# Optimization experiments

Measured on AMD Instinct MI355X. Metric: run time of the kernel, lower is better.

## Reference

```python
import jax, jax.numpy as jnp
from jax import lax
import numpy as np

IMG_CH = 3
C = 48            # total channels
HIDDEN = 256
FIRE_RATE = 0.5
DX_NOISE = 0.0
NEG_SLOPE = 0.01  # torch LeakyReLU default


def _dwconv(x_nchw, w):
    # depthwise 3x3 conv with reflect padding, w: [C,1,3,3]
    xp = jnp.pad(x_nchw, ((0, 0), (0, 0), (1, 1), (1, 1)), mode='reflect')
    return lax.conv_general_dilated(
        xp, w, window_strides=(1, 1), padding='VALID',
        feature_group_count=C,
        dimension_numbers=('NCHW', 'OIHW', 'NCHW'))


def setup_inputs() -> dict:
    key = jax.random.key(0)
    ks = jax.random.split(key, 6)
    x = jax.random.normal(ks[0], (8, 256, 256, C), dtype=jnp.float32)
    filt0 = jax.random.normal(ks[1], (C, 1, 3, 3), dtype=jnp.float32) * 0.1
    filt1 = jax.random.normal(ks[2], (C, 1, 3, 3), dtype=jnp.float32) * 0.1
    fan_in = 3 * C
    w1 = jax.random.normal(ks[3], (HIDDEN, 3 * C), dtype=jnp.float32) / np.sqrt(fan_in).astype(np.float32)
    b1 = jax.random.normal(ks[4], (HIDDEN,), dtype=jnp.float32) * 0.01
    # original zero-inits w2; randomized small so outputs/grads are nontrivial
    w2 = jax.random.normal(ks[5], (C, HIDDEN), dtype=jnp.float32) * 0.02
    return {"x": x, "filt0": filt0, "filt1": filt1, "w1": w1, "b1": b1, "w2": w2, "steps": 4}


def reference(x, filt0, filt1, w1, b1, w2, steps):
    ch_mask = (jnp.arange(C) >= IMG_CH).astype(x.dtype)  # immutable image channels
    rng = jax.random.key(42)
    for i in range(steps):
        xc = jnp.transpose(x, (0, 3, 1, 2))                       # [B,C,H,W]
        p = jnp.concatenate([xc, _dwconv(xc, filt0), _dwconv(xc, filt1)], axis=1)
        p = jnp.transpose(p, (0, 2, 3, 1))                        # [B,H,W,3C]
        h = jax.nn.leaky_relu(jnp.einsum('bhwf,of->bhwo', p, w1) + b1, NEG_SLOPE)
        d = jnp.einsum('bhwo,co->bhwc', h, w2)                    # [B,H,W,C]
        k1, k2 = jax.random.split(jax.random.fold_in(rng, i))
        fire = (jax.random.uniform(k1, d.shape[:3] + (1,)) > FIRE_RATE).astype(d.dtype)
        d = d * fire + DX_NOISE * jax.random.normal(k2, d.shape[:3] + (1,), dtype=d.dtype)
        d = d * ch_mask
        x = x + d
    return x
```

## Files before the change

kernel.cpp:

```cpp
#include <hip/hip_runtime.h>
#include <stdint.h>
#include <stddef.h>


#define B_   8
#define H_   256
#define W_   256
#define C_   48
#define F_   144
#define HID_ 256
#define PW_  64
#define NTOT (B_*H_*W_*C_)

typedef __attribute__((ext_vector_type(8))) short short8;
typedef __attribute__((ext_vector_type(4))) float f32x4;

struct U2 { unsigned x, y; };

__host__ __device__ __forceinline__ unsigned rotl32(unsigned v, int r) {
  return (v << r) | (v >> (32 - r));
}

__host__ __device__ __forceinline__ U2 threefry2x32(unsigned k0, unsigned k1,
                                                    unsigned x0, unsigned x1) {
  const unsigned k2 = k0 ^ k1 ^ 0x1BD11BDAu;
  x0 += k0; x1 += k1;
#define TF_R(r) { x0 += x1; x1 = rotl32(x1, r); x1 ^= x0; }
  TF_R(13) TF_R(15) TF_R(26) TF_R(6)
  x0 += k1; x1 += k2 + 1u;
  TF_R(17) TF_R(29) TF_R(16) TF_R(24)
  x0 += k2; x1 += k0 + 2u;
  TF_R(13) TF_R(15) TF_R(26) TF_R(6)
  x0 += k0; x1 += k1 + 3u;
  TF_R(17) TF_R(29) TF_R(16) TF_R(24)
  x0 += k1; x1 += k2 + 4u;
  TF_R(13) TF_R(15) TF_R(26) TF_R(6)
  x0 += k2; x1 += k0 + 5u;
#undef TF_R
  U2 r; r.x = x0; r.y = x1; return r;
}

__device__ __forceinline__ unsigned short f2bf(float f) {
  unsigned u = __float_as_uint(f);
  unsigned r = u + 0x7FFFu + ((u >> 16) & 1u);
  return (unsigned short)(r >> 16);
}
__device__ __forceinline__ unsigned packbf2(float lo, float hi) {
  return (unsigned)f2bf(lo) | ((unsigned)f2bf(hi) << 16);
}

#define W1B_N 40960
#define W2B_N 12288
__global__ void nca_pack(const float* __restrict__ w1,
                         const float* __restrict__ w2,
                         const float* __restrict__ f0,
                         const float* __restrict__ f1,
                         unsigned short* __restrict__ w1B,
                         unsigned short* __restrict__ w2B,
                         float4* __restrict__ ffp) {
  int i = blockIdx.x * 256 + threadIdx.x;
  if (i < W1B_N) {
    int nt = i / 2560, r = i - nt * 2560;
    int ks = r >> 9, r2 = r & 511;
    int lane = r2 >> 3, j = r2 & 7;
    int o = nt * 16 + (lane & 15);
    int f = ks * 32 + (lane >> 4) * 8 + j;
    w1B[i] = f2bf((f < F_) ? w1[o * F_ + f] : 0.0f);
  }
  if (i < W2B_N) {
    int nt = i >> 12, r = i & 4095;
    int ks = r >> 9, r2 = r & 511;
    int lane = r2 >> 3, j = r2 & 7;
    int c = nt * 16 + (lane & 15);
    int o = ks * 32 + (lane >> 4) * 8 + j;
    w2B[i] = f2bf(w2[c * HID_ + o]);
  }
  if (i < 216) {
    int cp = i / 9, tap = i - cp * 9;
    float4 v;
    v.x = f0[(2 * cp) * 9 + tap];     v.y = f0[(2 * cp + 1) * 9 + tap];
    v.z = f1[(2 * cp) * 9 + tap];     v.w = f1[(2 * cp + 1) * 9 + tap];
    ffp[i] = v;
  }
}

__global__ __launch_bounds__(256, 4)
void nca_step(const float* __restrict__ xin, float* __restrict__ xout,
              const float4* __restrict__ ffp,
              const unsigned short* __restrict__ w1B,
              const float* __restrict__ b1,
              const unsigned short* __restrict__ w2B,
              unsigned ka, unsigned kb) {
  __shared__ __align__(16) char smem[39488];
  __shared__ float fireL[PW_];
  short* xT = (short*)smem;
  short* pA = (short*)(smem + 19008);
  short* hA = (short*)smem;

  const int t = threadIdx.x;
  const int bid = blockIdx.x;
  const int wseg = bid & 3;
  const int h = (bid >> 2) & 255;
  const int b = bid >> 10;
  const int w0 = wseg * PW_;
  const int gbase = ((b * H_ + h) * W_ + w0) * C_;

  if (t < PW_) {
    unsigned j = (unsigned)((b * H_ + h) * W_ + w0 + t);
    U2 r = threefry2x32(ka, kb, 0u, j);
    unsigned bits = r.x ^ r.y;
    fireL[t] = ((bits >> 9) > 4194304u) ? 1.0f : 0.0f;
  } else if (t < 192) {
    int idx = t - 64;
    int mt = idx >> 5, lane = 32 + (idx & 31);
    short8 z = {};
    *(short8*)&pA[(((mt * 5 + 4) << 6) | lane) << 3] = z;
  }
  {
    const int hr[3] = { (h == 0) ? 1 : h - 1, h, (h == 255) ? 254 : h + 1 };
#pragma unroll
    for (int g = 0; g < 10; ++g) {
      int i = t + g * 256;
      if (i < 2376) {
        int row = i / 792, rem = i - row * 792;
        int px = rem / 12, c4 = rem - px * 12;
        int w = w0 - 1 + px;
        int wg = (w < 0) ? 1 : (w > 255) ? 254 : w;
        const float4 v = *(const float4*)&xin[((b * H_ + hr[row]) * W_ + wg) * C_ + c4 * 4];
        uint2 d; d.x = packbf2(v.x, v.y); d.y = packbf2(v.z, v.w);
        *(uint2*)&xT[(row * 66 + px) * 48 + c4 * 4] = d;
      }
    }
  }
  __syncthreads();

  if (t < 192) {
    const int cp = t >> 3, sub = t & 7;
    const int c = cp * 2;
    float4 ff[9];
#pragma unroll
    for (int tap = 0; tap < 9; ++tap) ff[tap] = ffp[cp * 9 + tap];
    unsigned* pA32 = (unsigned*)pA;
#pragma unroll
    for (int i = 0; i < 8; ++i) {
      const int p = sub + 8 * i;
      float a0x = 0.f, a0y = 0.f, a1x = 0.f, a1y = 0.f, cx = 0.f, cy = 0.f;
#pragma unroll
      for (int dy = 0; dy < 3; ++dy) {
#pragma unroll
        for (int dx = 0; dx < 3; ++dx) {
          unsigned d = *(const unsigned*)&xT[(dy * 66 + p + dx) * 48 + c];
          float lo = __uint_as_float(d << 16);
          float hi = __uint_as_float(d & 0xFFFF0000u);
          const float4 f = ff[dy * 3 + dx];
          a0x = fmaf(lo, f.x, a0x); a0y = fmaf(hi, f.y, a0y);
          a1x = fmaf(lo, f.z, a1x); a1y = fmaf(hi, f.w, a1y);
          if (dy == 1 && dx == 1) { cx = lo; cy = hi; }
        }
      }
      const int mt = p >> 4, pxl = p & 15;
#pragma unroll
      for (int seg = 0; seg < 3; ++seg) {
        int k = seg * 48 + c;
        int ks = k >> 5, q = (k & 31) >> 3, jw = (k & 7) >> 1;
        int lane2 = pxl + (q << 4);
        float lo = (seg == 0) ? cx : (seg == 1) ? a0x : a1x;
        float hi = (seg == 0) ? cy : (seg == 1) ? a0y : a1y;
        pA32[(((mt * 5 + ks) << 6) | lane2) * 4 + jw] = packbf2(lo, hi);
      }
    }
  }
  __syncthreads();

  const int wv = t >> 6, lane = t & 63;
  const int c16 = lane & 15, quad = lane >> 4;
  f32x4 acc[4][4];
#pragma unroll
  for (int mt = 0; mt < 4; ++mt)
#pragma unroll
    for (int nt = 0; nt < 4; ++nt) acc[mt][nt] = f32x4{0.f, 0.f, 0.f, 0.f};

#pragma unroll
  for (int ks = 0; ks < 5; ++ks) {
    short8 a[4];
#pragma unroll
    for (int mt = 0; mt < 4; ++mt)
      a[mt] = *(const short8*)&pA[(((mt * 5 + ks) << 6) | lane) << 3];
#pragma unroll
    for (int nt = 0; nt < 4; ++nt) {
      const int ntg = wv * 4 + nt;
      const short8 bf = *(const short8*)&w1B[(((ntg * 5 + ks) << 6) | lane) << 3];
#pragma unroll
      for (int mt = 0; mt < 4; ++mt)
        acc[mt][nt] = __builtin_amdgcn_mfma_f32_16x16x32_bf16(a[mt], bf, acc[mt][nt], 0, 0, 0);
    }
  }
  __syncthreads();

#pragma unroll
  for (int nt = 0; nt < 4; ++nt) {
    const int o = (wv * 4 + nt) * 16 + c16;
    const float bias = b1[o];
    const int ks2 = o >> 5, q2 = (o & 31) >> 3, j2 = o & 7;
#pragma unroll
    for (int mt = 0; mt < 4; ++mt) {
#pragma unroll
      for (int reg = 0; reg < 4; ++reg) {
        float z = acc[mt][nt][reg] + bias;
        z = (z >= 0.f) ? z : 0.01f * z;
        const int lane2 = (quad * 4 + reg) + (q2 << 4);
        hA[((((mt * 8 + ks2) << 6) | lane2) << 3) + j2] = (short)f2bf(z);
      }
    }
  }
  __syncthreads();

  {
    f32x4 acc2[3];
#pragma unroll
    for (int nt = 0; nt < 3; ++nt) acc2[nt] = f32x4{0.f, 0.f, 0.f, 0.f};
#pragma unroll
    for (int ks = 0; ks < 8; ++ks) {
      const short8 a2 = *(const short8*)&hA[(((wv * 8 + ks) << 6) | lane) << 3];
#pragma unroll
      for (int nt = 0; nt < 3; ++nt) {
        const short8 bf = *(const short8*)&w2B[(((nt * 8 + ks) << 6) | lane) << 3];
        acc2[nt] = __builtin_amdgcn_mfma_f32_16x16x32_bf16(a2, bf, acc2[nt], 0, 0, 0);
      }
    }
#pragma unroll
    for (int nt = 0; nt < 3; ++nt) {
      const int c = nt * 16 + c16;
#pragma unroll
      for (int reg = 0; reg < 4; ++reg) {
        const int pxl = wv * 16 + quad * 4 + reg;
        float d = acc2[nt][reg] * fireL[pxl];
        if (c < 3) d = 0.f;
        const int idx = gbase + pxl * C_ + c;
        xout[idx] = xin[idx] + d;
      }
    }
  }
}

extern "C" void kernel_launch(void* const* d_in, const int* in_sizes, int n_in,
                              void* d_out, int out_size, void* d_ws, size_t ws_size,
                              hipStream_t stream) {
  const float* xin = (const float*)d_in[0];
  const float* f0  = (const float*)d_in[1];
  const float* f1  = (const float*)d_in[2];
  const float* w1  = (const float*)d_in[3];
  const float* b1  = (const float*)d_in[4];
  const float* w2  = (const float*)d_in[5];
  float* xout = (float*)d_out;
  (void)in_sizes; (void)n_in; (void)out_size; (void)ws_size;

  unsigned ka[4], kb[4];
  for (int i = 0; i < 4; ++i) {
    U2 fold = threefry2x32(0u, 42u, 0u, (unsigned)i);
    U2 k1 = threefry2x32(fold.x, fold.y, 0u, 0u);
    ka[i] = k1.x; kb[i] = k1.y;
  }

  unsigned short* w1B = (unsigned short*)d_ws;
  unsigned short* w2B = w1B + W1B_N;
  float4* ffp = (float4*)((char*)d_ws + (W1B_N + W2B_N) * 2);
  float* bufA = (float*)((char*)d_ws + (W1B_N + W2B_N) * 2 + 216 * 16);

  const dim3 gs(B_ * H_ * (W_ / PW_));
  const dim3 bs(256);

  nca_pack<<<(W1B_N + 255) / 256, 256, 0, stream>>>(w1, w2, f0, f1, w1B, w2B, ffp);
  nca_step<<<gs, bs, 0, stream>>>(xin,  bufA, ffp, w1B, b1, w2B, ka[0], kb[0]);
  nca_step<<<gs, bs, 0, stream>>>(bufA, xout, ffp, w1B, b1, w2B, ka[1], kb[1]);
  nca_step<<<gs, bs, 0, stream>>>(xout, bufA, ffp, w1B, b1, w2B, ka[2], kb[2]);
  nca_step<<<gs, bs, 0, stream>>>(bufA, xout, ffp, w1B, b1, w2B, ka[3], kb[3]);
}
```

Measured before the change: 803.7 us.

## Fold depthwise convs into first GEMM and store intermediate state as bf16

The two depthwise 3x3 convolutions and the identity branch are folded algebraically into a 432-wide first-layer weight matrix. The MFMA now reads A fragments straight from the bf16 halo tile, which removes the separate conv stage, the pA staging buffer and one barrier. Intermediate step states are kept in bf16 in global memory (using d_out as scratch) to roughly halve read/write traffic between steps. The cost is nearly three times the MFMA work for layer one, plus precision loss from accumulating the state in bf16 across steps.

Result: slower. 875.6 us (+8.9%).

```diff
diff --git a/kernel.cpp b/kernel.cpp
--- a/kernel.cpp
+++ b/kernel.cpp
@@ -11,6 +11,7 @@
 #define HID_ 256
 #define PW_  64
 #define NTOT (B_*H_*W_*C_)
+#define XSTR 56
 
 typedef __attribute__((ext_vector_type(8))) short short8;
 typedef __attribute__((ext_vector_type(4))) float f32x4;
@@ -48,24 +49,33 @@
 __device__ __forceinline__ unsigned packbf2(float lo, float hi) {
   return (unsigned)f2bf(lo) | ((unsigned)f2bf(hi) << 16);
 }
-
-#define W1B_N 40960
+__device__ __forceinline__ float bf2f(unsigned short u) {
+  return __uint_as_float(((unsigned)u) << 16);
+}
+
+#define W1B_N 114688
 #define W2B_N 12288
 __global__ void nca_pack(const float* __restrict__ w1,
                          const float* __restrict__ w2,
                          const float* __restrict__ f0,
                          const float* __restrict__ f1,
                          unsigned short* __restrict__ w1B,
-                         unsigned short* __restrict__ w2B,
-                         float4* __restrict__ ffp) {
+                         unsigned short* __restrict__ w2B) {
   int i = blockIdx.x * 256 + threadIdx.x;
   if (i < W1B_N) {
-    int nt = i / 2560, r = i - nt * 2560;
+    int ntg = i / 7168, r = i - ntg * 7168;
     int ks = r >> 9, r2 = r & 511;
     int lane = r2 >> 3, j = r2 & 7;
-    int o = nt * 16 + (lane & 15);
-    int f = ks * 32 + (lane >> 4) * 8 + j;
-    w1B[i] = f2bf((f < F_) ? w1[o * F_ + f] : 0.0f);
+    int o = ntg * 16 + (lane & 15);
+    int k = ks * 32 + (lane >> 4) * 8 + j;
+    float v = 0.0f;
+    if (k < 432) {
+      int tap = k / 48, c = k - tap * 48;
+      v = w1[o * F_ + 48 + c] * f0[c * 9 + tap]
+        + w1[o * F_ + 96 + c] * f1[c * 9 + tap];
+      if (tap == 4) v += w1[o * F_ + c];
+    }
+    w1B[i] = f2bf(v);
   }
   if (i < W2B_N) {
     int nt = i >> 12, r = i & 4095;
@@ -75,26 +85,18 @@
     int o = ks * 32 + (lane >> 4) * 8 + j;
     w2B[i] = f2bf(w2[c * HID_ + o]);
   }
-  if (i < 216) {
-    int cp = i / 9, tap = i - cp * 9;
-    float4 v;
-    v.x = f0[(2 * cp) * 9 + tap];     v.y = f0[(2 * cp + 1) * 9 + tap];
-    v.z = f1[(2 * cp) * 9 + tap];     v.w = f1[(2 * cp + 1) * 9 + tap];
-    ffp[i] = v;
-  }
-}
-
+}
+
+template<int INBF, int OUTBF>
 __global__ __launch_bounds__(256, 4)
-void nca_step(const float* __restrict__ xin, float* __restrict__ xout,
-              const float4* __restrict__ ffp,
+void nca_step(const void* __restrict__ xin_, void* __restrict__ xout_,
               const unsigned short* __restrict__ w1B,
               const float* __restrict__ b1,
               const unsigned short* __restrict__ w2B,
               unsigned ka, unsigned kb) {
-  __shared__ __align__(16) char smem[39488];
+  __shared__ __align__(16) char smem[32768];
   __shared__ float fireL[PW_];
   short* xT = (short*)smem;
-  short* pA = (short*)(smem + 19008);
   short* hA = (short*)smem;
 
   const int t = threadIdx.x;
@@ -110,11 +112,6 @@
     U2 r = threefry2x32(ka, kb, 0u, j);
     unsigned bits = r.x ^ r.y;
     fireL[t] = ((bits >> 9) > 4194304u) ? 1.0f : 0.0f;
-  } else if (t < 192) {
-    int idx = t - 64;
-    int mt = idx >> 5, lane = 32 + (idx & 31);
-    short8 z = {};
-    *(short8*)&pA[(((mt * 5 + 4) << 6) | lane) << 3] = z;
   }
   {
     const int hr[3] = { (h == 0) ? 1 : h - 1, h, (h == 255) ? 254 : h + 1 };
@@ -126,47 +123,15 @@
         int px = rem / 12, c4 = rem - px * 12;
         int w = w0 - 1 + px;
         int wg = (w < 0) ? 1 : (w > 255) ? 254 : w;
-        const float4 v = *(const float4*)&xin[((b * H_ + hr[row]) * W_ + wg) * C_ + c4 * 4];
-        uint2 d; d.x = packbf2(v.x, v.y); d.y = packbf2(v.z, v.w);
-        *(uint2*)&xT[(row * 66 + px) * 48 + c4 * 4] = d;
-      }
-    }
-  }
-  __syncthreads();
-
-  if (t < 192) {
-    const int cp = t >> 3, sub = t & 7;
-    const int c = cp * 2;
-    float4 ff[9];
-#pragma unroll
-    for (int tap = 0; tap < 9; ++tap) ff[tap] = ffp[cp * 9 + tap];
-    unsigned* pA32 = (unsigned*)pA;
-#pragma unroll
-    for (int i = 0; i < 8; ++i) {
-      const int p = sub + 8 * i;
-      float a0x = 0.f, a0y = 0.f, a1x = 0.f, a1y = 0.f, cx = 0.f, cy = 0.f;
-#pragma unroll
-      for (int dy = 0; dy < 3; ++dy) {
-#pragma unroll
-        for (int dx = 0; dx < 3; ++dx) {
-          unsigned d = *(const unsigned*)&xT[(dy * 66 + p + dx) * 48 + c];
-          float lo = __uint_as_float(d << 16);
-          float hi = __uint_as_float(d & 0xFFFF0000u);
-          const float4 f = ff[dy * 3 + dx];
-          a0x = fmaf(lo, f.x, a0x); a0y = fmaf(hi, f.y, a0y);
-          a1x = fmaf(lo, f.z, a1x); a1y = fmaf(hi, f.w, a1y);
-          if (dy == 1 && dx == 1) { cx = lo; cy = hi; }
+        const int gidx = ((b * H_ + hr[row]) * W_ + wg) * C_ + c4 * 4;
+        uint2 d;
+        if constexpr (INBF) {
+          d = *(const uint2*)((const unsigned short*)xin_ + gidx);
+        } else {
+          const float4 v = *(const float4*)((const float*)xin_ + gidx);
+          d.x = packbf2(v.x, v.y); d.y = packbf2(v.z, v.w);
         }
-      }
-      const int mt = p >> 4, pxl = p & 15;
-#pragma unroll
-      for (int seg = 0; seg < 3; ++seg) {
-        int k = seg * 48 + c;
-        int ks = k >> 5, q = (k & 31) >> 3, jw = (k & 7) >> 1;
-        int lane2 = pxl + (q << 4);
-        float lo = (seg == 0) ? cx : (seg == 1) ? a0x : a1x;
-        float hi = (seg == 0) ? cy : (seg == 1) ? a0y : a1y;
-        pA32[(((mt * 5 + ks) << 6) | lane2) * 4 + jw] = packbf2(lo, hi);
+        *(uint2*)&xT[(row * 66 + px) * XSTR + c4 * 4] = d;
       }
     }
   }
@@ -181,15 +146,22 @@
     for (int nt = 0; nt < 4; ++nt) acc[mt][nt] = f32x4{0.f, 0.f, 0.f, 0.f};
 
 #pragma unroll
-  for (int ks = 0; ks < 5; ++ks) {
+  for (int ks = 0; ks < 14; ++ks) {
+    int chunk = ks * 4 + quad;
+    if (chunk > 53) chunk = 53;
+    const int tap = chunk / 6;
+    const int cst = (chunk - tap * 6) * 8;
+    const int dy = tap / 3;
+    const int dx = tap - dy * 3;
+    const int off0 = (dy * 66 + c16 + dx) * XSTR + cst;
     short8 a[4];
 #pragma unroll
     for (int mt = 0; mt < 4; ++mt)
-      a[mt] = *(const short8*)&pA[(((mt * 5 + ks) << 6) | lane) << 3];
+      a[mt] = *(const short8*)&xT[off0 + mt * (16 * XSTR)];
 #pragma unroll
     for (int nt = 0; nt < 4; ++nt) {
       const int ntg = wv * 4 + nt;
-      const short8 bf = *(const short8*)&w1B[(((ntg * 5 + ks) << 6) | lane) << 3];
+      const short8 bf = *(const short8*)&w1B[(((ntg * 14 + ks) << 6) | lane) << 3];
 #pragma unroll
       for (int mt = 0; mt < 4; ++mt)
         acc[mt][nt] = __builtin_amdgcn_mfma_f32_16x16x32_bf16(a[mt], bf, acc[mt][nt], 0, 0, 0);
@@ -237,7 +209,12 @@
         float d = acc2[nt][reg] * fireL[pxl];
         if (c < 3) d = 0.f;
         const int idx = gbase + pxl * C_ + c;
-        xout[idx] = xin[idx] + d;
+        float base;
+        if constexpr (INBF) base = bf2f(((const unsigned short*)xin_)[idx]);
+        else                base = ((const float*)xin_)[idx];
+        const float r = base + d;
+        if constexpr (OUTBF) ((unsigned short*)xout_)[idx] = f2bf(r);
+        else                 ((float*)xout_)[idx] = r;
       }
     }
   }
@@ -264,15 +241,15 @@
 
   unsigned short* w1B = (unsigned short*)d_ws;
   unsigned short* w2B = w1B + W1B_N;
-  float4* ffp = (float4*)((char*)d_ws + (W1B_N + W2B_N) * 2);
-  float* bufA = (float*)((char*)d_ws + (W1B_N + W2B_N) * 2 + 216 * 16);
+  unsigned short* xb  = (unsigned short*)((char*)d_ws + (size_t)(W1B_N + W2B_N) * 2);
+  unsigned short* ob  = (unsigned short*)d_out;
 
   const dim3 gs(B_ * H_ * (W_ / PW_));
   const dim3 bs(256);
 
-  nca_pack<<<(W1B_N + 255) / 256, 256, 0, stream>>>(w1, w2, f0, f1, w1B, w2B, ffp);
-  nca_step<<<gs, bs, 0, stream>>>(xin,  bufA, ffp, w1B, b1, w2B, ka[0], kb[0]);
-  nca_step<<<gs, bs, 0, stream>>>(bufA, xout, ffp, w1B, b1, w2B, ka[1], kb[1]);
-  nca_step<<<gs, bs, 0, stream>>>(xout, bufA, ffp, w1B, b1, w2B, ka[2], kb[2]);
-  nca_step<<<gs, bs, 0, stream>>>(bufA, xout, ffp, w1B, b1, w2B, ka[3], kb[3]);
-}
+  nca_pack<<<(W1B_N + 255) / 256, 256, 0, stream>>>(w1, w2, f0, f1, w1B, w2B);
+  nca_step<0, 1><<<gs, bs, 0, stream>>>(xin, xb,   w1B, b1, w2B, ka[0], kb[0]);
+  nca_step<1, 1><<<gs, bs, 0, stream>>>(xb,  ob,   w1B, b1, w2B, ka[1], kb[1]);
+  nca_step<1, 1><<<gs, bs, 0, stream>>>(ob,  xb,   w1B, b1, w2B, ka[2], kb[2]);
+  nca_step<1, 0><<<gs, bs, 0, stream>>>(xb,  xout, w1B, b1, w2B, ka[3], kb[3]);
+}
```
